# Kernel tuning notes

Hardware: AMD Instinct MI355X
Metric: run time of the kernel (lower is better)

Reference implementation:

```python
import jax, jax.numpy as jnp
import numpy as np

C = 512       # out_channels
RATIO = 2
K = C // RATIO          # init_channels = 256
NEW = K * (RATIO - 1)   # new_channels = 256
H = W = 160
EPS = 1e-5


def _conv(x, w, pad, groups=1):
    return jax.lax.conv_general_dilated(
        x, w, (1, 1), [(pad, pad), (pad, pad)],
        dimension_numbers=("NCHW", "OIHW", "NCHW"),
        feature_group_count=groups)


def _bn(x, g, b, m, v):
    scale = (g / jnp.sqrt(v + EPS))[None, :, None, None]
    return (x - m[None, :, None, None]) * scale + b[None, :, None, None]


def setup_inputs() -> dict:
    key = jax.random.key(0)
    ks = jax.random.split(key, 16)
    s = 0.05
    return {
        "x": jax.random.normal(ks[0], (1, C, H, W), jnp.float32),
        "w_fc1": jax.random.normal(ks[1], (K, C), jnp.float32) * s,
        "w_fc2": jax.random.normal(ks[2], (C, K), jnp.float32) * s,
        "w_cheap": jax.random.normal(ks[3], (NEW, 1, 3, 3), jnp.float32) * s,  # depthwise, groups=K
        "bn1_g": jnp.ones((NEW,), jnp.float32),
        "bn1_b": jnp.zeros((NEW,), jnp.float32),
        "bn1_m": jax.random.normal(ks[4], (NEW,), jnp.float32) * s,
        "bn1_v": jax.random.uniform(ks[5], (NEW,), jnp.float32, 0.5, 1.5),
        "w_dc1": jax.random.normal(ks[6], (C, 2 * C, 1, 1), jnp.float32) * s,
        "b_dc1": jax.random.normal(ks[7], (C,), jnp.float32) * s,
        "bn2_g": jnp.ones((C,), jnp.float32),
        "bn2_b": jnp.zeros((C,), jnp.float32),
        "bn2_m": jax.random.normal(ks[8], (C,), jnp.float32) * s,
        "bn2_v": jax.random.uniform(ks[9], (C,), jnp.float32, 0.5, 1.5),
        "w_dc2": jax.random.normal(ks[10], (C, C, 3, 3), jnp.float32) * s,
        "b_dc2": jax.random.normal(ks[11], (C,), jnp.float32) * s,
    }


def reference(x, w_fc1, w_fc2, w_cheap, bn1_g, bn1_b, bn1_m, bn1_v,
              w_dc1, b_dc1, bn2_g, bn2_b, bn2_m, bn2_v, w_dc2, b_dc2):
    # ---- channel attention (CBAM-style shared MLP over avg+max pool) ----
    avg = x.mean(axis=(2, 3))                      # [1, C]
    mx = x.max(axis=(2, 3))                        # [1, C]
    mlp = lambda p: jax.nn.relu(p @ w_fc1.T) @ w_fc2.T
    scales = jax.nn.sigmoid(mlp(avg) + mlp(mx))    # [1, C]
    # ---- sort-based top-K channel select, kept in channel-index order ----
    # torch: sort desc, drop channels ranked >= K via boolean mask (mask is in
    # channel-index order), equivalent to gathering sorted top-K indices.
    _, top_idx = jax.lax.top_k(scales[0], K)
    idx = jnp.sort(top_idx)
    x1 = x[:, idx]                                 # [1, K, H, W]
    # ---- cheap operation: depthwise 3x3 + BN + ReLU ----
    x2 = jax.nn.relu(_bn(_conv(x1, w_cheap, 1, groups=K), bn1_g, bn1_b, bn1_m, bn1_v))
    # ---- concat [x*scales, x1, x2] -> 2C channels ----
    cat = jnp.concatenate([x * scales[:, :, None, None], x1, x2], axis=1)
    # ---- down_channel: 1x1 conv + BN + 3x3 conv + ReLU ----
    h = _conv(cat, w_dc1, 0) + b_dc1[None, :, None, None]
    h = _bn(h, bn2_g, bn2_b, bn2_m, bn2_v)
    h = _conv(h, w_dc2, 1) + b_dc2[None, :, None, None]
    return jax.nn.relu(h)
```

## Files before the change

kernel.cpp:

```cpp
#include <hip/hip_runtime.h>
#include <math.h>

#define C 512
#define K 256
#define HW 160
#define NPIX (HW*HW)
#define PW 162
#define EPS 1e-5f

typedef __attribute__((ext_vector_type(8))) short s16x8;
typedef __attribute__((ext_vector_type(16))) float f32x16;

__device__ __forceinline__ unsigned short f2bf(float f) {
    unsigned int u = __float_as_uint(f);
    u += 0x7fffu + ((u >> 16) & 1u);
    return (unsigned short)(u >> 16);
}

__device__ __forceinline__ void ldg_lds16(const void* g, void* l) {
    __builtin_amdgcn_global_load_lds((const __attribute__((address_space(1))) unsigned int*)g,
                                     (__attribute__((address_space(3))) unsigned int*)l, 16, 0, 0);
}

#define WAIT_VM0()  asm volatile("s_waitcnt vmcnt(0)" ::: "memory")
#define WAIT_LGKM0() asm volatile("s_waitcnt lgkmcnt(0)" ::: "memory")

__global__ void reduce_kernel(const float* __restrict__ x,
                              float* __restrict__ avg, float* __restrict__ mx) {
    int c = blockIdx.x;
    const float4* xc = (const float4*)(x + (size_t)c * NPIX);
    float s = 0.f, m = -INFINITY;
    for (int p = threadIdx.x; p < NPIX / 4; p += 256) {
        float4 v = xc[p];
        s += v.x + v.y + v.z + v.w;
        m = fmaxf(m, fmaxf(fmaxf(v.x, v.y), fmaxf(v.z, v.w)));
    }
    __shared__ float ss[256], sm[256];
    ss[threadIdx.x] = s; sm[threadIdx.x] = m;
    __syncthreads();
    for (int o = 128; o > 0; o >>= 1) {
        if (threadIdx.x < o) {
            ss[threadIdx.x] += ss[threadIdx.x + o];
            sm[threadIdx.x] = fmaxf(sm[threadIdx.x], sm[threadIdx.x + o]);
        }
        __syncthreads();
    }
    if (threadIdx.x == 0) {
        avg[c] = ss[0] / (float)NPIX;
        mx[c]  = sm[0];
    }
}

__global__ void mlp_select_kernel(const float* __restrict__ avg,
                                  const float* __restrict__ mx,
                                  const float* __restrict__ w_fc1,
                                  const float* __restrict__ w_fc2,
                                  float* __restrict__ scales_out,
                                  int* __restrict__ idx,
                                  int* __restrict__ pos) {
    __shared__ float s_avg[C], s_mx[C], s_h[K], s_scales[C];
    __shared__ int s_sel[C];
    int t = threadIdx.x;
    s_avg[t] = avg[t];
    s_mx[t]  = mx[t];
    __syncthreads();
    if (t < K) {
        float ha = 0.f, hm = 0.f;
        const float4* wr = (const float4*)(w_fc1 + (size_t)t * C);
        for (int c = 0; c < C / 4; c++) {
            float4 w = wr[c];
            ha += s_avg[4*c]*w.x + s_avg[4*c+1]*w.y + s_avg[4*c+2]*w.z + s_avg[4*c+3]*w.w;
            hm += s_mx[4*c]*w.x + s_mx[4*c+1]*w.y + s_mx[4*c+2]*w.z + s_mx[4*c+3]*w.w;
        }
        s_h[t] = fmaxf(ha, 0.f) + fmaxf(hm, 0.f);
    }
    __syncthreads();
    {
        float o = 0.f;
        const float4* wr = (const float4*)(w_fc2 + (size_t)t * K);
        for (int k = 0; k < K / 4; k++) {
            float4 w = wr[k];
            o += s_h[4*k]*w.x + s_h[4*k+1]*w.y + s_h[4*k+2]*w.z + s_h[4*k+3]*w.w;
        }
        float sc = 1.f / (1.f + expf(-o));
        s_scales[t] = sc;
        scales_out[t] = sc;
    }
    __syncthreads();
    {
        float v = s_scales[t];
        int rank = 0;
        for (int i = 0; i < C; i++) {
            float u = s_scales[i];
            rank += (u > v) || (u == v && i < t);
        }
        s_sel[t] = (rank < K) ? 1 : 0;
    }
    __syncthreads();
    {
        int p = 0;
        for (int i = 0; i < t; i++) p += s_sel[i];
        if (s_sel[t]) { idx[p] = t; pos[t] = p; }
        else pos[t] = -1;
    }
}

__global__ void prep_kernel(const float* __restrict__ w_dc2, unsigned short* __restrict__ w3,
                            const float* __restrict__ w_dc1, const float* __restrict__ scales,
                            const int* __restrict__ pos, unsigned short* __restrict__ wA,
                            unsigned short* __restrict__ hpad,
                            const float* __restrict__ b_dc1,
                            const float* __restrict__ g2, const float* __restrict__ b2,
                            const float* __restrict__ m2, const float* __restrict__ v2,
                            float* __restrict__ scale2, float* __restrict__ shift2) {
    int b = blockIdx.x;
    if (b < 4608) {
        int t = b >> 9, co = b & 511;
        for (int ci = threadIdx.x; ci < 512; ci += 256)
            w3[((size_t)t * 512 + co) * 512 + ci] = f2bf(w_dc2[((size_t)co * 512 + ci) * 9 + t]);
    } else if (b < 5120) {
        int co = b - 4608;
        const float* wr = w_dc1 + (size_t)co * 1024;
        for (int c = threadIdx.x; c < 768; c += 256) {
            float v;
            if (c < 512) {
                v = wr[c] * scales[c];
                int pp = pos[c];
                if (pp >= 0) v += wr[512 + pp];
            } else {
                v = wr[768 + (c - 512)];
            }
            wA[(size_t)co * 768 + c] = f2bf(v);
        }
    } else if (b < 5281) {
        int t = (b - 5120) * 256 + threadIdx.x;
        int pix = t >> 6;
        int p;
        if (pix < 162)      p = pix;
        else if (pix < 324) p = 161 * PW + (pix - 162);
        else {
            int r = pix - 324;
            p = (1 + (r >> 1)) * PW + ((r & 1) ? 161 : 0);
        }
        *(uint4*)&hpad[(size_t)p * 512 + (t & 63) * 8] = make_uint4(0u, 0u, 0u, 0u);
    } else {
        for (int c = threadIdx.x; c < C; c += 256) {
            float s = g2[c] * rsqrtf(v2[c] + EPS);
            scale2[c] = s;
            shift2[c] = (b_dc1[c] - m2[c]) * s + b2[c];
        }
    }
}

__global__ void dw_t_kernel(const float* __restrict__ x,
                            const int* __restrict__ idx,
                            const float* __restrict__ wch,
                            const float* __restrict__ g1, const float* __restrict__ b1,
                            const float* __restrict__ m1, const float* __restrict__ v1,
                            unsigned short* __restrict__ xcat) {
    __shared__ float tile[32][33];
    int tx = threadIdx.x & 31, ty = threadIdx.x >> 5;
    int pbase = blockIdx.x * 32, kbase = blockIdx.y * 32;
    int y = pbase / HW, x0 = pbase % HW;
    int px = x0 + tx;
#pragma unroll
    for (int jj = 0; jj < 4; jj++) {
        int k = kbase + ty + jj * 8;
        int c = idx[k];
        const float* xc = x + (size_t)c * NPIX;
        const float* wk = wch + k * 9;
        float acc = 0.f;
#pragma unroll
        for (int dy = 0; dy < 3; dy++) {
            int yy = y + dy - 1;
            if (yy < 0 || yy >= HW) continue;
#pragma unroll
            for (int dx = 0; dx < 3; dx++) {
                int xv = px + dx - 1;
                if (xv < 0 || xv >= HW) continue;
                acc += xc[yy * HW + xv] * wk[dy * 3 + dx];
            }
        }
        float s = g1[k] * rsqrtf(v1[k] + EPS);
        tile[ty + jj * 8][tx] = fmaxf((acc - m1[k]) * s + b1[k], 0.f);
    }
    __syncthreads();
#pragma unroll
    for (int jj = 0; jj < 4; jj++) {
        int p = pbase + ty + jj * 8;
        xcat[(size_t)p * 768 + 512 + kbase + tx] = f2bf(tile[tx][ty + jj * 8]);
    }
}

__global__ void transpose_kernel(const float* __restrict__ x,
                                 unsigned short* __restrict__ xcat) {
    __shared__ float tile[32][33];
    int tx = threadIdx.x & 31, ty = threadIdx.x >> 5;
    int pbase = blockIdx.x * 32, cbase = blockIdx.y * 32;
#pragma unroll
    for (int j = 0; j < 4; j++) {
        int c = cbase + ty + j * 8;
        tile[ty + j * 8][tx] = x[(size_t)c * NPIX + pbase + tx];
    }
    __syncthreads();
#pragma unroll
    for (int j = 0; j < 4; j++) {
        int p = pbase + ty + j * 8;
        xcat[(size_t)p * 768 + cbase + tx] = f2bf(tile[tx][ty + j * 8]);
    }
}

__global__ __launch_bounds__(64, 1) void conv1_mfma(const unsigned short* __restrict__ xcat,
        const unsigned short* __restrict__ wA,
        const float* __restrict__ scale2, const float* __restrict__ shift2,
        unsigned short* __restrict__ hpad) {
    __shared__ unsigned short Al[2][640 * 8];
    __shared__ unsigned short Bl[2][256 * 8];
    int y = blockIdx.x, co0 = blockIdx.y * 64;
    int lane = threadIdx.x;
    int l31 = lane & 31, q = lane >> 5;
    f32x16 acc[5][2] = {};

    int aoff[10], boff[4];
#pragma unroll
    for (int r = 0; r < 10; r++) {
        int g = r * 64 + lane;
        int px = g >> 2, jg = (g & 3) ^ ((px >> 1) & 3);
        aoff[r] = px * 768 + jg * 8;
    }
#pragma unroll
    for (int r = 0; r < 4; r++) {
        int g = r * 64 + lane;
        int co = g >> 2, jg = (g & 3) ^ ((co >> 1) & 3);
        boff[r] = co * 768 + jg * 8;
    }
    int raoff[2];
#pragma unroll
    for (int s = 0; s < 2; s++)
        raoff[s] = l31 * 64 + (((s * 2 + q) ^ ((l31 >> 1) & 3)) << 4);
    const unsigned short* arow = xcat + (size_t)y * HW * 768;
    const unsigned short* brow = wA + (size_t)co0 * 768;

#pragma unroll
    for (int r = 0; r < 10; r++) ldg_lds16(arow + aoff[r], &Al[0][r * 512]);
#pragma unroll
    for (int r = 0; r < 4; r++)  ldg_lds16(brow + boff[r], &Bl[0][r * 512]);

    for (int ph = 0; ph < 24; ph++) {
        const unsigned short* Ar = Al[ph & 1];
        const unsigned short* Br = Bl[ph & 1];
        WAIT_VM0();
        s16x8 af[5][2], bf[2][2];
#pragma unroll
        for (int s = 0; s < 2; s++) {
#pragma unroll
            for (int i = 0; i < 5; i++)
                af[i][s] = *(const s16x8*)((const char*)Ar + i * 2048 + raoff[s]);
#pragma unroll
            for (int j = 0; j < 2; j++)
                bf[j][s] = *(const s16x8*)((const char*)Br + j * 2048 + raoff[s]);
        }
        WAIT_LGKM0();
        if (ph < 23) {
            int kc = (ph + 1) * 32;
            unsigned short* An = Al[(ph + 1) & 1];
            unsigned short* Bn = Bl[(ph + 1) & 1];
#pragma unroll
            for (int r = 0; r < 10; r++) ldg_lds16(arow + kc + aoff[r], &An[r * 512]);
#pragma unroll
            for (int r = 0; r < 4; r++)  ldg_lds16(brow + kc + boff[r], &Bn[r * 512]);
        }
#pragma unroll
        for (int s = 0; s < 2; s++)
#pragma unroll
            for (int i = 0; i < 5; i++)
#pragma unroll
                for (int j = 0; j < 2; j++)
                    acc[i][j] = __builtin_amdgcn_mfma_f32_32x32x16_bf16(af[i][s], bf[j][s], acc[i][j], 0, 0, 0);
    }
#pragma unroll
    for (int j = 0; j < 2; j++) {
        int co = co0 + j * 32 + l31;
        float s2 = scale2[co], sh = shift2[co];
#pragma unroll
        for (int i = 0; i < 5; i++) {
#pragma unroll
            for (int rg = 0; rg < 4; rg++) {
#pragma unroll
                for (int t = 0; t < 4; t++) {
                    int px = i * 32 + t + rg * 8 + q * 4;
                    size_t pp = (size_t)(y + 1) * PW + px + 1;
                    hpad[pp * 512 + co] = f2bf(acc[i][j][rg * 4 + t] * s2 + sh);
                }
            }
        }
    }
}

__global__ __launch_bounds__(64, 1) void conv3_mfma(const unsigned short* __restrict__ hpad,
        const unsigned short* __restrict__ w3,
        const float* __restrict__ bias, float* __restrict__ out) {
    __shared__ unsigned short Al[2][648 * 8];
    __shared__ unsigned short Bl[2][768 * 8];
    int y = blockIdx.x, co0 = blockIdx.y * 64;
    int lane = threadIdx.x;
    int l31 = lane & 31, q = lane >> 5;
    f32x16 acc[5][2] = {};

    int aoff[11], boff[12];
#pragma unroll
    for (int r = 0; r < 11; r++) {
        int g = r * 64 + lane;
        int px = g >> 2, jg = (g & 3) ^ ((px >> 1) & 3);
        aoff[r] = px * 512 + jg * 8;
    }
#pragma unroll
    for (int r = 0; r < 12; r++) {
        int g = r * 64 + lane;
        int tt = g >> 8, co = (g >> 2) & 63, jg = (g & 3) ^ ((co >> 1) & 3);
        boff[r] = (tt * 512 + co) * 512 + jg * 8;
    }
    int raoff[3][2], rboff[2];
#pragma unroll
    for (int dx = 0; dx < 3; dx++)
#pragma unroll
        for (int s = 0; s < 2; s++) {
            int m = l31 + dx;
            raoff[dx][s] = m * 64 + ((((s * 2 + q)) ^ ((m >> 1) & 3)) << 4);
        }
#pragma unroll
    for (int s = 0; s < 2; s++)
        rboff[s] = l31 * 64 + (((s * 2 + q) ^ ((l31 >> 1) & 3)) << 4);

    auto stage = [&](int ph, int buf) {
        int dy = ph >> 4, kc = (ph & 15) * 32;
        const unsigned short* ab = hpad + ((size_t)(y + dy) * PW) * 512 + kc;
        unsigned short* An = Al[buf];
#pragma unroll
        for (int r = 0; r < 10; r++) ldg_lds16(ab + aoff[r], &An[r * 512]);
        if (lane < 8)                ldg_lds16(ab + aoff[10], &An[10 * 512]);
        const unsigned short* bb = w3 + ((size_t)(dy * 3) * 512 + co0) * 512 + kc;
        unsigned short* Bn = Bl[buf];
#pragma unroll
        for (int r = 0; r < 12; r++) ldg_lds16(bb + boff[r], &Bn[r * 512]);
    };

    stage(0, 0);
    for (int ph = 0; ph < 48; ph++) {
        const unsigned short* Ar = Al[ph & 1];
        const unsigned short* Br = Bl[ph & 1];
        WAIT_VM0();
        s16x8 af[3][5][2], bf[3][2][2];
#pragma unroll
        for (int dx = 0; dx < 3; dx++) {
#pragma unroll
            for (int s = 0; s < 2; s++) {
#pragma unroll
                for (int i = 0; i < 5; i++)
                    af[dx][i][s] = *(const s16x8*)((const char*)Ar + i * 2048 + raoff[dx][s]);
#pragma unroll
                for (int j = 0; j < 2; j++)
                    bf[dx][j][s] = *(const s16x8*)((const char*)Br + dx * 4096 + j * 2048 + rboff[s]);
            }
        }
        WAIT_LGKM0();
        if (ph < 47) stage(ph + 1, (ph + 1) & 1);
#pragma unroll
        for (int dx = 0; dx < 3; dx++)
#pragma unroll
            for (int s = 0; s < 2; s++)
#pragma unroll
                for (int i = 0; i < 5; i++)
#pragma unroll
                    for (int j = 0; j < 2; j++)
                        acc[i][j] = __builtin_amdgcn_mfma_f32_32x32x16_bf16(af[dx][i][s], bf[dx][j][s], acc[i][j], 0, 0, 0);
    }
#pragma unroll
    for (int j = 0; j < 2; j++) {
        int co = co0 + j * 32 + l31;
        float b = bias[co];
        float* op = out + (size_t)co * NPIX + y * HW;
#pragma unroll
        for (int i = 0; i < 5; i++) {
#pragma unroll
            for (int rg = 0; rg < 4; rg++) {
                int px = i * 32 + rg * 8 + q * 4;
                float4 v;
                v.x = fmaxf(acc[i][j][rg * 4 + 0] + b, 0.f);
                v.y = fmaxf(acc[i][j][rg * 4 + 1] + b, 0.f);
                v.z = fmaxf(acc[i][j][rg * 4 + 2] + b, 0.f);
                v.w = fmaxf(acc[i][j][rg * 4 + 3] + b, 0.f);
                *(float4*)&op[px] = v;
            }
        }
    }
}

extern "C" void kernel_launch(void* const* d_in, const int* in_sizes, int n_in,
                              void* d_out, int out_size, void* d_ws, size_t ws_size,
                              hipStream_t stream) {
    const float* x      = (const float*)d_in[0];
    const float* w_fc1  = (const float*)d_in[1];
    const float* w_fc2  = (const float*)d_in[2];
    const float* w_ch   = (const float*)d_in[3];
    const float* bn1_g  = (const float*)d_in[4];
    const float* bn1_b  = (const float*)d_in[5];
    const float* bn1_m  = (const float*)d_in[6];
    const float* bn1_v  = (const float*)d_in[7];
    const float* w_dc1  = (const float*)d_in[8];
    const float* b_dc1  = (const float*)d_in[9];
    const float* bn2_g  = (const float*)d_in[10];
    const float* bn2_b  = (const float*)d_in[11];
    const float* bn2_m  = (const float*)d_in[12];
    const float* bn2_v  = (const float*)d_in[13];
    const float* w_dc2  = (const float*)d_in[14];
    const float* b_dc2  = (const float*)d_in[15];
    float* out = (float*)d_out;

    char* ws = (char*)d_ws;
    float* avg    = (float*)(ws + 0);
    float* mx     = (float*)(ws + 2048);
    float* scales = (float*)(ws + 4096);
    int*   idx    = (int*)  (ws + 6144);
    int*   pos    = (int*)  (ws + 7168);
    float* scale2 = (float*)(ws + 9216);
    float* shift2 = (float*)(ws + 11264);
    unsigned short* wA   = (unsigned short*)(ws + 16384);
    unsigned short* w3   = (unsigned short*)(ws + 802816);
    unsigned short* xcat = (unsigned short*)(ws + 31735808);
    unsigned short* hpad = (unsigned short*)(ws + 71057408);

    reduce_kernel<<<C, 256, 0, stream>>>(x, avg, mx);
    mlp_select_kernel<<<1, C, 0, stream>>>(avg, mx, w_fc1, w_fc2, scales, idx, pos);
    prep_kernel<<<5282, 256, 0, stream>>>(w_dc2, w3, w_dc1, scales, pos, wA, hpad,
                                          b_dc1, bn2_g, bn2_b, bn2_m, bn2_v, scale2, shift2);
    dw_t_kernel<<<dim3(800, 8), 256, 0, stream>>>(x, idx, w_ch, bn1_g, bn1_b, bn1_m, bn1_v, xcat);
    transpose_kernel<<<dim3(800, 16), 256, 0, stream>>>(x, xcat);
    conv1_mfma<<<dim3(HW, 8), 64, 0, stream>>>(xcat, wA, scale2, shift2, hpad);
    conv3_mfma<<<dim3(HW, 8), 64, 0, stream>>>(hpad, w3, b_dc2, out);
}
```

Baseline: 451.5 us.

## Triple-buffer LDS pipelines in both MFMA convs and stage weight transpose through LDS

Both the 1x1 and 3x3 MFMA conv kernels move from double to triple LDS buffering. Global-to-LDS loads are issued two K-phases ahead, and a partial vmcnt wait replaces the full drain, so memory latency overlaps more MFMA work. Fragment registers are now loaded per sub-step instead of all at once, which lowers register pressure but interleaves LDS reads with compute. The prep kernel now reads each output channel's 3x3 weights contiguously into LDS before transposing, instead of doing strided global reads, which cuts its grid from 5282 to 1186 blocks. The hardcoded vmcnt values (14 and 23) depend on the exact number of loads issued per stage.

Measured after the change: 531.6 us. 1.18x slower.

```diff
diff --git a/kernel.cpp b/kernel.cpp
--- a/kernel.cpp
+++ b/kernel.cpp
@@ -22,8 +22,9 @@
                                      (__attribute__((address_space(3))) unsigned int*)l, 16, 0, 0);
 }
 
-#define WAIT_VM0()  asm volatile("s_waitcnt vmcnt(0)" ::: "memory")
-#define WAIT_LGKM0() asm volatile("s_waitcnt lgkmcnt(0)" ::: "memory")
+#define WAIT_VM0()   asm volatile("s_waitcnt vmcnt(0)" ::: "memory")
+#define WAIT_VM14()  asm volatile("s_waitcnt vmcnt(14)" ::: "memory")
+#define WAIT_VM23()  asm volatile("s_waitcnt vmcnt(23)" ::: "memory")
 
 __global__ void reduce_kernel(const float* __restrict__ x,
                               float* __restrict__ avg, float* __restrict__ mx) {
@@ -113,13 +114,20 @@
                             const float* __restrict__ g2, const float* __restrict__ b2,
                             const float* __restrict__ m2, const float* __restrict__ v2,
                             float* __restrict__ scale2, float* __restrict__ shift2) {
+    __shared__ unsigned short lw[4608];
     int b = blockIdx.x;
-    if (b < 4608) {
-        int t = b >> 9, co = b & 511;
-        for (int ci = threadIdx.x; ci < 512; ci += 256)
-            w3[((size_t)t * 512 + co) * 512 + ci] = f2bf(w_dc2[((size_t)co * 512 + ci) * 9 + t]);
-    } else if (b < 5120) {
-        int co = b - 4608;
+    if (b < 512) {
+        int co = b;
+        const float* src = w_dc2 + (size_t)co * 4608;
+        for (int u = threadIdx.x; u < 4608; u += 256)
+            lw[u] = f2bf(src[u]);
+        __syncthreads();
+        for (int u = threadIdx.x; u < 4608; u += 256) {
+            int t = u >> 9, ci = u & 511;
+            w3[((size_t)t * 512 + co) * 512 + ci] = lw[ci * 9 + t];
+        }
+    } else if (b < 1024) {
+        int co = b - 512;
         const float* wr = w_dc1 + (size_t)co * 1024;
         for (int c = threadIdx.x; c < 768; c += 256) {
             float v;
@@ -132,8 +140,8 @@
             }
             wA[(size_t)co * 768 + c] = f2bf(v);
         }
-    } else if (b < 5281) {
-        int t = (b - 5120) * 256 + threadIdx.x;
+    } else if (b < 1185) {
+        int t = (b - 1024) * 256 + threadIdx.x;
         int pix = t >> 6;
         int p;
         if (pix < 162)      p = pix;
@@ -214,8 +222,8 @@
         const unsigned short* __restrict__ wA,
         const float* __restrict__ scale2, const float* __restrict__ shift2,
         unsigned short* __restrict__ hpad) {
-    __shared__ unsigned short Al[2][640 * 8];
-    __shared__ unsigned short Bl[2][256 * 8];
+    __shared__ unsigned short Al[3][640 * 8];
+    __shared__ unsigned short Bl[3][256 * 8];
     int y = blockIdx.x, co0 = blockIdx.y * 64;
     int lane = threadIdx.x;
     int l31 = lane & 31, q = lane >> 5;
@@ -241,42 +249,38 @@
     const unsigned short* arow = xcat + (size_t)y * HW * 768;
     const unsigned short* brow = wA + (size_t)co0 * 768;
 
-#pragma unroll
-    for (int r = 0; r < 10; r++) ldg_lds16(arow + aoff[r], &Al[0][r * 512]);
-#pragma unroll
-    for (int r = 0; r < 4; r++)  ldg_lds16(brow + boff[r], &Bl[0][r * 512]);
-
+    auto stage = [&](int ph, int buf) {
+        int kc = ph * 32;
+        unsigned short* An = Al[buf];
+        unsigned short* Bn = Bl[buf];
+#pragma unroll
+        for (int r = 0; r < 10; r++) ldg_lds16(arow + kc + aoff[r], &An[r * 512]);
+#pragma unroll
+        for (int r = 0; r < 4; r++)  ldg_lds16(brow + kc + boff[r], &Bn[r * 512]);
+    };
+
+    stage(0, 0);
+    stage(1, 1);
     for (int ph = 0; ph < 24; ph++) {
-        const unsigned short* Ar = Al[ph & 1];
-        const unsigned short* Br = Bl[ph & 1];
-        WAIT_VM0();
-        s16x8 af[5][2], bf[2][2];
+        const unsigned short* Ar = Al[ph % 3];
+        const unsigned short* Br = Bl[ph % 3];
+        if (ph == 23) { WAIT_VM0(); } else { WAIT_VM14(); }
 #pragma unroll
         for (int s = 0; s < 2; s++) {
+            s16x8 af[5], bf[2];
 #pragma unroll
             for (int i = 0; i < 5; i++)
-                af[i][s] = *(const s16x8*)((const char*)Ar + i * 2048 + raoff[s]);
+                af[i] = *(const s16x8*)((const char*)Ar + i * 2048 + raoff[s]);
 #pragma unroll
             for (int j = 0; j < 2; j++)
-                bf[j][s] = *(const s16x8*)((const char*)Br + j * 2048 + raoff[s]);
-        }
-        WAIT_LGKM0();
-        if (ph < 23) {
-            int kc = (ph + 1) * 32;
-            unsigned short* An = Al[(ph + 1) & 1];
-            unsigned short* Bn = Bl[(ph + 1) & 1];
-#pragma unroll
-            for (int r = 0; r < 10; r++) ldg_lds16(arow + kc + aoff[r], &An[r * 512]);
-#pragma unroll
-            for (int r = 0; r < 4; r++)  ldg_lds16(brow + kc + boff[r], &Bn[r * 512]);
-        }
-#pragma unroll
-        for (int s = 0; s < 2; s++)
+                bf[j] = *(const s16x8*)((const char*)Br + j * 2048 + raoff[s]);
+            if (s == 0 && ph < 22) stage(ph + 2, (ph + 2) % 3);
 #pragma unroll
             for (int i = 0; i < 5; i++)
 #pragma unroll
                 for (int j = 0; j < 2; j++)
-                    acc[i][j] = __builtin_amdgcn_mfma_f32_32x32x16_bf16(af[i][s], bf[j][s], acc[i][j], 0, 0, 0);
+                    acc[i][j] = __builtin_amdgcn_mfma_f32_32x32x16_bf16(af[i], bf[j], acc[i][j], 0, 0, 0);
+        }
     }
 #pragma unroll
     for (int j = 0; j < 2; j++) {
@@ -300,8 +304,8 @@
 __global__ __launch_bounds__(64, 1) void conv3_mfma(const unsigned short* __restrict__ hpad,
         const unsigned short* __restrict__ w3,
         const float* __restrict__ bias, float* __restrict__ out) {
-    __shared__ unsigned short Al[2][648 * 8];
-    __shared__ unsigned short Bl[2][768 * 8];
+    __shared__ unsigned short Al[3][648 * 8];
+    __shared__ unsigned short Bl[3][768 * 8];
     int y = blockIdx.x, co0 = blockIdx.y * 64;
     int lane = threadIdx.x;
     int l31 = lane & 31, q = lane >> 5;
@@ -346,34 +350,32 @@
     };
 
     stage(0, 0);
+    stage(1, 1);
     for (int ph = 0; ph < 48; ph++) {
-        const unsigned short* Ar = Al[ph & 1];
-        const unsigned short* Br = Bl[ph & 1];
-        WAIT_VM0();
-        s16x8 af[3][5][2], bf[3][2][2];
+        const unsigned short* Ar = Al[ph % 3];
+        const unsigned short* Br = Bl[ph % 3];
+        if (ph == 47) { WAIT_VM0(); } else { WAIT_VM23(); }
 #pragma unroll
         for (int dx = 0; dx < 3; dx++) {
+            s16x8 af[5][2], bf[2][2];
 #pragma unroll
             for (int s = 0; s < 2; s++) {
 #pragma unroll
                 for (int i = 0; i < 5; i++)
-                    af[dx][i][s] = *(const s16x8*)((const char*)Ar + i * 2048 + raoff[dx][s]);
+                    af[i][s] = *(const s16x8*)((const char*)Ar + i * 2048 + raoff[dx][s]);
 #pragma unroll
                 for (int j = 0; j < 2; j++)
-                    bf[dx][j][s] = *(const s16x8*)((const char*)Br + dx * 4096 + j * 2048 + rboff[s]);
+                    bf[j][s] = *(const s16x8*)((const char*)Br + dx * 4096 + j * 2048 + rboff[s]);
             }
-        }
-        WAIT_LGKM0();
-        if (ph < 47) stage(ph + 1, (ph + 1) & 1);
-#pragma unroll
-        for (int dx = 0; dx < 3; dx++)
+            if (dx == 0 && ph < 46) stage(ph + 2, (ph + 2) % 3);
 #pragma unroll
             for (int s = 0; s < 2; s++)
 #pragma unroll
                 for (int i = 0; i < 5; i++)
 #pragma unroll
                     for (int j = 0; j < 2; j++)
-                        acc[i][j] = __builtin_amdgcn_mfma_f32_32x32x16_bf16(af[dx][i][s], bf[dx][j][s], acc[i][j], 0, 0, 0);
+                        acc[i][j] = __builtin_amdgcn_mfma_f32_32x32x16_bf16(af[i][s], bf[j][s], acc[i][j], 0, 0, 0);
+        }
     }
 #pragma unroll
     for (int j = 0; j < 2; j++) {
@@ -432,7 +434,7 @@
 
     reduce_kernel<<<C, 256, 0, stream>>>(x, avg, mx);
     mlp_select_kernel<<<1, C, 0, stream>>>(avg, mx, w_fc1, w_fc2, scales, idx, pos);
-    prep_kernel<<<5282, 256, 0, stream>>>(w_dc2, w3, w_dc1, scales, pos, wA, hpad,
+    prep_kernel<<<1186, 256, 0, stream>>>(w_dc2, w3, w_dc1, scales, pos, wA, hpad,
                                           b_dc1, bn2_g, bn2_b, bn2_m, bn2_v, scale2, shift2);
     dw_t_kernel<<<dim3(800, 8), 256, 0, stream>>>(x, idx, w_ch, bn1_g, bn1_b, bn1_m, bn1_v, xcat);
     transpose_kernel<<<dim3(800, 16), 256, 0, stream>>>(x, xcat);
```
